# Performance work log

Measured on AMD Instinct MI355X. Metric: run time of the kernel, lower is better.

The kernel has to match this reference:

```python
import jax, jax.numpy as jnp
import numpy as np

EPS_NORM = 1e-6
CLAMP_HI = 1.0 - 1e-6
NEG_INF = -1e30


def _cbrt_pos(x):
    # numerically safe x**(1/3) for x >= 0 (matches exp2(log2(x)/3) in the kernel)
    safe = jnp.where(x > 0, x, 1.0)
    return jnp.where(x > 0, safe ** (1.0 / 3.0), 0.0)


def _pow23_pos(x):
    # relu(x)**(2/3), safe at 0 (matches exp2(log2(max(x,0))*2/3))
    y = jnp.maximum(x, 0.0)
    safe = jnp.where(y > 0, y, 1.0)
    return jnp.where(y > 0, safe ** (2.0 / 3.0), 0.0)


def setup_inputs() -> dict:
    key = jax.random.key(0)
    kq, kk, kv, ks, kd = jax.random.split(key, 5)
    b, h, hkv, s, d = 2, 32, 8, 1024, 64
    return {
        "q": jax.random.normal(kq, (b, h, s, d), dtype=jnp.float32),
        "k": jax.random.normal(kk, (b, hkv, s, d), dtype=jnp.float32),
        "v": jax.random.normal(kv, (b, hkv, s, d), dtype=jnp.float32),
        "src": jax.random.normal(ks, (b, hkv, s), dtype=jnp.float32),
        "dest": jax.random.normal(kd, (b, hkv, s), dtype=jnp.float32),
    }


def reference(q, k, v, src, dest):
    # Preprocessing exactly as in chunked_decay():
    kn = k / (jnp.sqrt(jnp.sum(k * k, axis=-1, keepdims=True)) + EPS_NORM)
    s_gate = _cbrt_pos(jax.nn.sigmoid(src))    # sigmoid(src)**(1/3), [b,hk,S]
    d_gate = _cbrt_pos(jax.nn.sigmoid(dest))   # sigmoid(dest)**(1/3), [b,hk,S]

    # affinity[i,j] = relu(k_i . k_j)**(2/3) * dest_i**(1/3) * src_j**(1/3)
    aff = _pow23_pos(jnp.einsum("bhid,bhjd->bhij", kn, kn))
    aff = aff * d_gate[..., :, None] * s_gate[..., None, :]

    # per-pair log decay, strictly lower-triangular (i > j, as in the kernel mask)
    logdec = jnp.log1p(-jnp.clip(aff, 0.0, CLAMP_HI))
    S = q.shape[2]
    idx = jnp.arange(S)
    strict = idx[:, None] > idx[None, :]
    logdec = jnp.where(strict, logdec, 0.0)

    # cumulative decay seen by query i for key j: sum over j < i' < i (exclusive cumsum over i)
    D = jnp.cumsum(logdec, axis=2) - logdec  # [b,hk,S_i,S_j]

    # GQA: expand kv heads to query heads
    g = q.shape[1] // k.shape[1]
    kq_ = jnp.repeat(kn, g, axis=1)
    vq_ = jnp.repeat(v, g, axis=1)
    Dq_ = jnp.repeat(D, g, axis=1)

    # decay-gated causal softmax attention: logits = q.k + cumulative log-decay
    logits = jnp.einsum("bhid,bhjd->bhij", q, kq_) + Dq_
    causal = idx[:, None] >= idx[None, :]
    logits = jnp.where(causal, logits, NEG_INF)
    att = jax.nn.softmax(logits, axis=-1)
    out = jnp.einsum("bhij,bhjd->bhid", att, vq_)
    return out
```

## Files before the change

### kernel.cpp

```cpp
#include <hip/hip_runtime.h>
#include <hip/hip_bf16.h>
#include <math.h>

#define S_LEN 1024
#define DH 64
#define NB 2
#define NHQ 32
#define NHKV 8
#define NHEADS (NB*NHKV)
#define NTILE 16
#define NTRI 136
#define NEG_INF -1e30f
#define LOG2E 1.44269504088896340736f

using bf16x8 = __attribute__((ext_vector_type(8))) __bf16;
using f32x4  = __attribute__((ext_vector_type(4))) float;
using ushort4_t = __attribute__((ext_vector_type(4))) unsigned short;

__device__ inline unsigned short f2bf(float f){
  unsigned int u = __float_as_uint(f);
  unsigned int r = (u + 0x7FFFu + ((u >> 16) & 1u)) >> 16;
  return (unsigned short)r;
}
__device__ inline unsigned short f2bf_hw(float f){
  return __builtin_bit_cast(unsigned short, __float2bfloat16(f));
}

__device__ inline void gload16(const void* g, void* l){
  __builtin_amdgcn_global_load_lds(
      (const __attribute__((address_space(1))) void*)g,
      (__attribute__((address_space(3))) void*)l, 16, 0, 0);
}

__global__ __launch_bounds__(256) void k_prep(const float* __restrict__ q,
                                              const float* __restrict__ k,
                                              const float* __restrict__ v,
                                              const float* __restrict__ src,
                                              const float* __restrict__ dest,
                                              unsigned short* __restrict__ qb,
                                              unsigned short* __restrict__ knb,
                                              unsigned short* __restrict__ vT,
                                              float* __restrict__ sg,
                                              float* __restrict__ dg){
  __shared__ float tile[64][65];
  int bid = blockIdx.x;
  if (bid < 4096){
    int base = (bid*256 + threadIdx.x)*4;
    float4 qv = *(const float4*)(q + base);
    ushort4_t o;
    o[0] = f2bf_hw(qv.x*LOG2E); o[1] = f2bf_hw(qv.y*LOG2E);
    o[2] = f2bf_hw(qv.z*LOG2E); o[3] = f2bf_hw(qv.w*LOG2E);
    *(ushort4_t*)(qb + base) = o;
  } else if (bid < 4128){
    int e = ((bid - 4096)*256 + threadIdx.x)*4;
    if (e < NHEADS*S_LEN){
      float4 dv = *(const float4*)(dest + e);
      float4 og;
      #pragma unroll
      for (int i = 0; i < 4; ++i){
        float x = (i==0)?dv.x:(i==1)?dv.y:(i==2)?dv.z:dv.w;
        float s = 1.f/(1.f + __expf(-x));
        float g = (s > 0.f) ? exp2f(log2f(s)*(1.f/3.f)) : 0.f;
        if (i==0) og.x=g; else if (i==1) og.y=g; else if (i==2) og.z=g; else og.w=g;
      }
      *(float4*)(dg + e) = og;
    } else {
      int e2 = e - NHEADS*S_LEN;
      float4 sv = *(const float4*)(src + e2);
      float4 og;
      #pragma unroll
      for (int i = 0; i < 4; ++i){
        float x = (i==0)?sv.x:(i==1)?sv.y:(i==2)?sv.z:sv.w;
        float s = 1.f/(1.f + __expf(-x));
        float g = (s > 0.f) ? exp2f(log2f(s)*(1.f/3.f)) : 0.f;
        if (i==0) og.x=g; else if (i==1) og.y=g; else if (i==2) og.z=g; else og.w=g;
      }
      *(float4*)(sg + e2) = og;
    }
  } else if (bid < 8224){
    int row  = (bid - 4128)*4 + (threadIdx.x >> 6);
    int lane = threadIdx.x & 63;
    size_t idx = (size_t)row*DH + lane;
    float x = k[idx];
    float ss = x*x;
    #pragma unroll
    for (int off = 32; off > 0; off >>= 1) ss += __shfl_xor(ss, off);
    float r = x / (sqrtf(ss) + 1e-6f);
    knb[idx] = f2bf(r);
  } else {
    int vb = bid - 8224;
    int bh = vb >> 4;
    int jt = vb & 15;
    int j0 = jt*64;
    int tid = threadIdx.x;
    int c = tid & 63, r4 = tid >> 6;
    const float* vbp = v + ((size_t)bh << 16);
    #pragma unroll
    for (int p = 0; p < 16; ++p){
      int j = p*4 + r4;
      tile[j][c] = vbp[(size_t)(j0 + j)*DH + c];
    }
    __syncthreads();
    unsigned short* ob = vT + ((size_t)bh << 16);
    #pragma unroll
    for (int p = 0; p < 16; ++p){
      int dd = p*4 + r4;
      ob[(size_t)dd*S_LEN + j0 + c] = f2bf_hw(tile[c][dd]);
    }
  }
}

__global__ __launch_bounds__(256) void k_t16(const unsigned short* __restrict__ knh,
                                             const float* __restrict__ dg,
                                             const float* __restrict__ sg,
                                             float* __restrict__ T16){
  __shared__ unsigned short Ah[4096], Bh[4096];
  int head = blockIdx.x / NTRI;
  int t    = blockIdx.x % NTRI;
  int ti = 0;
  while ((ti+1)*(ti+2)/2 <= t) ti++;
  int tj = t - ti*(ti+1)/2;
  int i0 = ti*64, j0 = tj*64;
  const unsigned short* Hp = knh + (size_t)head*S_LEN*DH;
  int w = threadIdx.x >> 6, lane = threadIdx.x & 63;
  int g16 = lane >> 4, l16 = lane & 15;

  int rsub = lane >> 3;
  int cisw = ((lane & 7) ^ rsub) * 8;
  int s0 = (w*8 + rsub)*64   + cisw;
  int s1 = ((w+4)*8 + rsub)*64 + cisw;
  int l0 = w*512, l1 = (w+4)*512;
  {
    const unsigned short* ha = Hp + (size_t)i0*DH;
    gload16(ha + s0, Ah + l0);  gload16(ha + s1, Ah + l1);
    if (ti != tj){
      const unsigned short* hb = Hp + (size_t)j0*DH;
      gload16(hb + s0, Bh + l0);  gload16(hb + s1, Bh + l1);
    }
  }
  __syncthreads();
  const unsigned short* bhp = (ti == tj) ? Ah : Bh;

  int c0 = g16 ^ (l16 & 7);
  int e0 = l16*64 + c0*8;
  int e1 = l16*64 + (c0 ^ 4)*8;

  bf16x8 ah[2];
  ah[0] = *(const bf16x8*)(Ah + w*1024 + e0);
  ah[1] = *(const bf16x8*)(Ah + w*1024 + e1);

  f32x4 sc[4];
  #pragma unroll
  for (int n = 0; n < 4; ++n) sc[n] = (f32x4){0.f,0.f,0.f,0.f};
  #pragma unroll
  for (int n = 0; n < 4; ++n){
    bf16x8 bh0 = *(const bf16x8*)(bhp + n*1024 + e0);
    bf16x8 bh1 = *(const bf16x8*)(bhp + n*1024 + e1);
    sc[n] = __builtin_amdgcn_mfma_f32_16x16x32_bf16(ah[0], bh0, sc[n], 0, 0, 0);
    sc[n] = __builtin_amdgcn_mfma_f32_16x16x32_bf16(ah[1], bh1, sc[n], 0, 0, 0);
  }

  float dgv[4], sgv[4];
  #pragma unroll
  for (int r = 0; r < 4; ++r) dgv[r] = dg[head*S_LEN + i0 + w*16 + g16*4 + r];
  #pragma unroll
  for (int n = 0; n < 4; ++n) sgv[n] = sg[head*S_LEN + j0 + n*16 + l16];

  float tot[4];
  #pragma unroll
  for (int n = 0; n < 4; ++n){
    float s = 0.f;
    #pragma unroll
    for (int r = 0; r < 4; ++r){
      int gi = i0 + w*16 + g16*4 + r;
      int gj = j0 + n*16 + l16;
      float x = sc[n][r];
      float aff = (x > 0.f) ? exp2f(__log2f(x)*(2.f/3.f)) : 0.f;
      aff *= dgv[r]*sgv[n];
      float ld = __log2f(1.f - fminf(aff, 1.0f - 1e-6f));
      s += (gi > gj) ? ld : 0.f;
    }
    tot[n] = s;
  }
  float wt[4];
  #pragma unroll
  for (int n = 0; n < 4; ++n){
    float t0 = __shfl(tot[n], l16);
    float t1 = __shfl(tot[n], 16 + l16);
    float t2 = __shfl(tot[n], 32 + l16);
    float t3 = __shfl(tot[n], 48 + l16);
    wt[n] = t0 + t1 + t2 + t3;
  }
  float sel = (g16 == 0) ? wt[0] : (g16 == 1) ? wt[1] : (g16 == 2) ? wt[2] : wt[3];
  T16[((size_t)head*64 + ti*4 + w)*S_LEN + j0 + g16*16 + l16] = sel;
}

__global__ __launch_bounds__(256) void k_cpre16(const float* __restrict__ T16,
                                                float* __restrict__ Cpre16){
  __shared__ float tot[4][64];
  int head = blockIdx.x >> 4;
  int cb   = blockIdx.x & 15;
  int c    = threadIdx.x >> 6;
  int ci   = threadIdx.x & 63;
  int col  = cb*64 + ci;
  int tjc  = cb;
  float loc[16];
  float run = 0.f;
  #pragma unroll
  for (int i = 0; i < 16; ++i){
    int gg = c*16 + i;
    loc[i] = run;
    if ((gg >> 2) >= tjc) run += T16[((size_t)head*64 + gg)*S_LEN + col];
  }
  tot[c][ci] = run;
  __syncthreads();
  float base = 0.f;
  #pragma unroll
  for (int cc = 0; cc < 3; ++cc)
    if (cc < c) base += tot[cc][ci];
  #pragma unroll
  for (int i = 0; i < 16; ++i){
    int gg = c*16 + i;
    Cpre16[((size_t)head*64 + gg)*S_LEN + col] = base + loc[i];
  }
}

__global__ __launch_bounds__(256, 3) void k_attn(const unsigned short* __restrict__ qb,
                                              const unsigned short* __restrict__ knb,
                                              const unsigned short* __restrict__ vT,
                                              const float* __restrict__ Cpre16,
                                              const float* __restrict__ dg,
                                              const float* __restrict__ sg,
                                              float* __restrict__ out){
  __shared__ unsigned short kts[2][4096];
  __shared__ unsigned short vts[2][4096];
  __shared__ unsigned short plds[4096];
  __shared__ float biasT[2][64][20];

  int xcd   = blockIdx.x & 7;
  int inner = blockIdx.x >> 3;
  int kv    = (xcd << 1) | (inner & 1);
  int i16   = 63 - (inner >> 1);
  int w     = threadIdx.x >> 6;
  int lane  = threadIdx.x & 63;
  int g16 = lane >> 4, l16 = lane & 15;
  int i0   = i16*16;
  int njt  = (i16 >> 2) + 1;
  int head = kv;
  int b = kv >> 3, gh = kv & 7;
  int bh = b*32 + gh*4 + w;

  const unsigned short* Kp = knb + (size_t)head*S_LEN*DH;
  const unsigned short* Vp = vT  + (size_t)head*DH*S_LEN;
  const unsigned short* Qp = qb  + ((size_t)bh*S_LEN + i0)*DH;
  const float*          Cp = Cpre16 + ((size_t)head*64 + i16)*S_LEN;

  int rsub = lane >> 3;
  int cisw = ((lane & 7) ^ rsub) * 8;
  int kg0 = (w*8 + rsub)*64   + cisw;
  int kg1 = ((w+4)*8 + rsub)*64 + cisw;
  int vg0 = (w*8 + rsub)*1024 + cisw;
  int vg1 = ((w+4)*8 + rsub)*1024 + cisw;
  int kl0 = w*512;
  int kl1 = (w+4)*512;

  int c0 = g16 ^ (l16 & 7);
  int e0 = l16*64 + c0*8;
  int e1 = l16*64 + (c0 ^ 4)*8;
  int hi = l16 >> 3, lo = l16 & 7;
  unsigned short* pw = plds + w*1024;

  unsigned short* pp[16];
  #pragma unroll
  for (int n = 0; n < 4; ++n)
    #pragma unroll
    for (int r = 0; r < 4; ++r){
      int row = g16*4 + r;
      pp[n*4 + r] = pw + row*64 + (((2*n + hi) ^ (row & 7))*8) + lo;
    }

  bf16x8 aq[2];
  aq[0] = *(const bf16x8*)(Qp + (size_t)l16*DH + g16*8);
  aq[1] = *(const bf16x8*)(Qp + (size_t)l16*DH + 32 + g16*8);
  bf16x8 ahK[2];
  {
    size_t ro = (size_t)(i0 + l16)*DH + g16*8;
    ahK[0] = *(const bf16x8*)(Kp + ro);
    ahK[1] = *(const bf16x8*)(Kp + ro + 32);
  }
  float dgw[4];
  #pragma unroll
  for (int r = 0; r < 4; ++r) dgw[r] = dg[head*S_LEN + i0 + g16*4 + r];

  auto STAGE = [&](int bb, int jtile){
    const unsigned short* ks = Kp + (size_t)jtile*(64*DH);
    const unsigned short* vs = Vp + (size_t)jtile*64;
    gload16(ks + kg0, &kts[bb][kl0]);
    gload16(ks + kg1, &kts[bb][kl1]);
    gload16(vs + vg0, &vts[bb][kl0]);
    gload16(vs + vg1, &vts[bb][kl1]);
  };

  auto BIAS = [&](int jt, int buf){
    int colw = jt*64 + (w << 4) + l16;
    float sgv_o = sg[head*S_LEN + colw];
    float cp_o  = Cp[colw];
    const unsigned short* hrow = Kp + (size_t)colw*DH;
    bf16x8 bh0 = *(const bf16x8*)(hrow + g16*8);
    bf16x8 bh1 = *(const bf16x8*)(hrow + 32 + g16*8);
    f32x4 bd = (f32x4){0.f,0.f,0.f,0.f};
    bd = __builtin_amdgcn_mfma_f32_16x16x32_bf16(ahK[0], bh0, bd, 0, 0, 0);
    bd = __builtin_amdgcn_mfma_f32_16x16x32_bf16(ahK[1], bh1, bd, 0, 0, 0);
    float pre[4];
    float s = 0.f;
    #pragma unroll
    for (int r = 0; r < 4; ++r){
      float x = bd[r];
      float aff = (x > 0.f) ? exp2f(__log2f(x)*(2.f/3.f)) : 0.f;
      aff *= dgw[r]*sgv_o;
      float ld = __log2f(1.f - fminf(aff, 1.0f - 1e-6f));
      ld = ((i0 + g16*4 + r) > colw) ? ld : 0.f;
      pre[r] = s; s += ld;
    }
    float t0 = __shfl(s, l16);
    float t1 = __shfl(s, 16 + l16);
    float t2 = __shfl(s, 32 + l16);
    float offg = (g16 > 0 ? t0 : 0.f) + (g16 > 1 ? t1 : 0.f) + (g16 > 2 ? t2 : 0.f);
    f32x4 st;
    #pragma unroll
    for (int r = 0; r < 4; ++r) st[r] = cp_o + offg + pre[r];
    *(f32x4*)&biasT[buf][(w << 4) + l16][g16*4] = st;
  };

  f32x4 oacc[4];
  float m[4], ssum[4];
  #pragma unroll
  for (int n = 0; n < 4; ++n) oacc[n] = (f32x4){0.f,0.f,0.f,0.f};
  #pragma unroll
  for (int r = 0; r < 4; ++r){ m[r] = NEG_INF; ssum[r] = 0.f; }

  auto SM_PV = [&](f32x4* sc, const unsigned short* vcur){
    float mx[4];
    #pragma unroll
    for (int r = 0; r < 4; ++r)
      mx[r] = fmaxf(fmaxf(sc[0][r], sc[1][r]), fmaxf(sc[2][r], sc[3][r]));
    #pragma unroll
    for (int off = 8; off >= 1; off >>= 1)
      #pragma unroll
      for (int r = 0; r < 4; ++r)
        mx[r] = fmaxf(mx[r], __shfl_xor(mx[r], off));
    float dmax = fmaxf(fmaxf(mx[0]-m[0], mx[1]-m[1]), fmaxf(mx[2]-m[2], mx[3]-m[3]));
    if (__any(dmax > 8.f)){
      #pragma unroll
      for (int r = 0; r < 4; ++r){
        float mn = fmaxf(m[r], mx[r]);
        float scale = exp2f(m[r] - mn);
        m[r] = mn;
        ssum[r] *= scale;
        #pragma unroll
        for (int n = 0; n < 4; ++n) oacc[n][r] *= scale;
      }
    }
    #pragma unroll
    for (int n = 0; n < 4; ++n){
      #pragma unroll
      for (int r = 0; r < 4; ++r){
        float pv = exp2f(sc[n][r] - m[r]);
        ssum[r] += pv;
        *pp[n*4 + r] = f2bf_hw(pv);
      }
    }
    bf16x8 pa0 = *(const bf16x8*)(pw + e0);
    bf16x8 pa1 = *(const bf16x8*)(pw + e1);
    __builtin_amdgcn_s_setprio(1);
    #pragma unroll
    for (int n = 0; n < 4; ++n){
      bf16x8 bv = *(const bf16x8*)(vcur + n*1024 + e0);
      oacc[n] = __builtin_amdgcn_mfma_f32_16x16x32_bf16(pa0, bv, oacc[n], 0, 0, 0);
    }
    #pragma unroll
    for (int n = 0; n < 4; ++n){
      bf16x8 bv = *(const bf16x8*)(vcur + n*1024 + e1);
      oacc[n] = __builtin_amdgcn_mfma_f32_16x16x32_bf16(pa1, bv, oacc[n], 0, 0, 0);
    }
    __builtin_amdgcn_s_setprio(0);
  };

  STAGE(0, 0);
  BIAS(0, 0);
  __syncthreads();

  int cur = 0, nb = 0;
  for (int jt = 0; jt < njt - 1; ++jt){
    const unsigned short* kcur = &kts[cur][0];
    const unsigned short* vcur = &vts[cur][0];

    STAGE(cur ^ 1, jt + 1);

    f32x4 sc[4];
    #pragma unroll
    for (int n = 0; n < 4; ++n) sc[n] = (f32x4){0.f,0.f,0.f,0.f};
    __builtin_amdgcn_s_setprio(1);
    #pragma unroll
    for (int n = 0; n < 4; ++n){
      bf16x8 bk0 = *(const bf16x8*)(kcur + n*1024 + e0);
      bf16x8 bk1 = *(const bf16x8*)(kcur + n*1024 + e1);
      sc[n] = __builtin_amdgcn_mfma_f32_16x16x32_bf16(aq[0], bk0, sc[n], 0, 0, 0);
      sc[n] = __builtin_amdgcn_mfma_f32_16x16x32_bf16(aq[1], bk1, sc[n], 0, 0, 0);
    }
    __builtin_amdgcn_s_setprio(0);

    BIAS(jt + 1, nb ^ 1);

    #pragma unroll
    for (int n = 0; n < 4; ++n){
      f32x4 bvv = *(const f32x4*)&biasT[nb][n*16 + l16][g16*4];
      #pragma unroll
      for (int r = 0; r < 4; ++r) sc[n][r] += bvv[r];
    }

    SM_PV(sc, vcur);

    __syncthreads();
    cur ^= 1; nb ^= 1;
  }

  {
    const unsigned short* kcur = &kts[cur][0];
    const unsigned short* vcur = &vts[cur][0];

    f32x4 sc[4];
    #pragma unroll
    for (int n = 0; n < 4; ++n) sc[n] = (f32x4){0.f,0.f,0.f,0.f};
    __builtin_amdgcn_s_setprio(1);
    #pragma unroll
    for (int n = 0; n < 4; ++n){
      bf16x8 bk0 = *(const bf16x8*)(kcur + n*1024 + e0);
      bf16x8 bk1 = *(const bf16x8*)(kcur + n*1024 + e1);
      sc[n] = __builtin_amdgcn_mfma_f32_16x16x32_bf16(aq[0], bk0, sc[n], 0, 0, 0);
      sc[n] = __builtin_amdgcn_mfma_f32_16x16x32_bf16(aq[1], bk1, sc[n], 0, 0, 0);
    }
    __builtin_amdgcn_s_setprio(0);

    int lim = (i16 & 3) << 4;
    #pragma unroll
    for (int n = 0; n < 4; ++n){
      f32x4 bvv = *(const f32x4*)&biasT[nb][n*16 + l16][g16*4];
      #pragma unroll
      for (int r = 0; r < 4; ++r){
        int row = g16*4 + r;
        int col = n*16 + l16;
        sc[n][r] = (col <= lim + row) ? (sc[n][r] + bvv[r]) : NEG_INF;
      }
    }

    SM_PV(sc, vcur);
  }

  #pragma unroll
  for (int off = 8; off >= 1; off >>= 1)
    #pragma unroll
    for (int r = 0; r < 4; ++r) ssum[r] += __shfl_xor(ssum[r], off);
  float* Op = out + ((size_t)bh*S_LEN + i0)*DH;
  #pragma unroll
  for (int n = 0; n < 4; ++n)
    #pragma unroll
    for (int r = 0; r < 4; ++r)
      Op[(size_t)(g16*4 + r)*DH + n*16 + l16] = oacc[n][r] / ssum[r];
}

extern "C" void kernel_launch(void* const* d_in, const int* in_sizes, int n_in,
                              void* d_out, int out_size, void* d_ws, size_t ws_size,
                              hipStream_t stream){
  const float* q    = (const float*)d_in[0];
  const float* k    = (const float*)d_in[1];
  const float* v    = (const float*)d_in[2];
  const float* src  = (const float*)d_in[3];
  const float* dest = (const float*)d_in[4];
  float* out = (float*)d_out;

  char* w = (char*)d_ws;
  unsigned short* qb   = (unsigned short*)w;
  unsigned short* knb  = (unsigned short*)(w + (size_t)(8u  << 20));
  unsigned short* vT   = (unsigned short*)(w + (size_t)(10u << 20));
  float*          dg   = (float*)(w + (size_t)(12u << 20));
  float*          sg   = (float*)(w + (size_t)(12u << 20) + 65536);
  float*          T16  = (float*)(w + (size_t)(13u << 20));
  float*          Cpre = (float*)(w + (size_t)(17u << 20));

  k_prep   <<<dim3(8480), dim3(256), 0, stream>>>(q, k, v, src, dest, qb, knb, vT, sg, dg);
  k_t16    <<<dim3(NHEADS*NTRI), dim3(256), 0, stream>>>(knb, dg, sg, T16);
  k_cpre16 <<<dim3(NHEADS*16), dim3(256), 0, stream>>>(T16, Cpre);
  k_attn   <<<dim3(NB*NHKV*64), dim3(256), 0, stream>>>(qb, knb, vT, Cpre, dg, sg, out);
}
```

Baseline: 70.87 us.

## Single-buffer K tile with extra barrier and swizzle bias LDS layout

After: 71.24 us. About the same (+0.5%).

```diff
diff --git a/kernel.cpp b/kernel.cpp
--- a/kernel.cpp
+++ b/kernel.cpp
@@ -232,10 +232,10 @@
                                               const float* __restrict__ dg,
                                               const float* __restrict__ sg,
                                               float* __restrict__ out){
-  __shared__ unsigned short kts[2][4096];
+  __shared__ unsigned short kts[4096];
   __shared__ unsigned short vts[2][4096];
   __shared__ unsigned short plds[4096];
-  __shared__ float biasT[2][64][20];
+  __shared__ float biasT[2][64][16];
 
   int xcd   = blockIdx.x & 7;
   int inner = blockIdx.x >> 3;
@@ -269,6 +269,7 @@
   int e1 = l16*64 + (c0 ^ 4)*8;
   int hi = l16 >> 3, lo = l16 & 7;
   unsigned short* pw = plds + w*1024;
+  int bsw = (g16 ^ (l16 & 3)) << 2;
 
   unsigned short* pp[16];
   #pragma unroll
@@ -292,11 +293,13 @@
   #pragma unroll
   for (int r = 0; r < 4; ++r) dgw[r] = dg[head*S_LEN + i0 + g16*4 + r];
 
-  auto STAGE = [&](int bb, int jtile){
+  auto STAGE_K = [&](int jtile){
     const unsigned short* ks = Kp + (size_t)jtile*(64*DH);
+    gload16(ks + kg0, kts + kl0);
+    gload16(ks + kg1, kts + kl1);
+  };
+  auto STAGE_V = [&](int bb, int jtile){
     const unsigned short* vs = Vp + (size_t)jtile*64;
-    gload16(ks + kg0, &kts[bb][kl0]);
-    gload16(ks + kg1, &kts[bb][kl1]);
     gload16(vs + vg0, &vts[bb][kl0]);
     gload16(vs + vg1, &vts[bb][kl1]);
   };
@@ -329,7 +332,7 @@
     f32x4 st;
     #pragma unroll
     for (int r = 0; r < 4; ++r) st[r] = cp_o + offg + pre[r];
-    *(f32x4*)&biasT[buf][(w << 4) + l16][g16*4] = st;
+    *(f32x4*)&biasT[buf][(w << 4) + l16][bsw] = st;
   };
 
   f32x4 oacc[4];
@@ -386,16 +389,17 @@
     __builtin_amdgcn_s_setprio(0);
   };
 
-  STAGE(0, 0);
+  STAGE_K(0);
+  STAGE_V(0, 0);
   BIAS(0, 0);
   __syncthreads();
 
   int cur = 0, nb = 0;
-  for (int jt = 0; jt < njt - 1; ++jt){
-    const unsigned short* kcur = &kts[cur][0];
+  for (int jt = 0; jt < njt; ++jt){
+    bool last = (jt == njt - 1);
     const unsigned short* vcur = &vts[cur][0];
 
-    STAGE(cur ^ 1, jt + 1);
+    if (!last) STAGE_V(cur ^ 1, jt + 1);
 
     f32x4 sc[4];
     #pragma unroll
@@ -403,58 +407,45 @@
     __builtin_amdgcn_s_setprio(1);
     #pragma unroll
     for (int n = 0; n < 4; ++n){
-      bf16x8 bk0 = *(const bf16x8*)(kcur + n*1024 + e0);
-      bf16x8 bk1 = *(const bf16x8*)(kcur + n*1024 + e1);
+      bf16x8 bk0 = *(const bf16x8*)(kts + n*1024 + e0);
+      bf16x8 bk1 = *(const bf16x8*)(kts + n*1024 + e1);
       sc[n] = __builtin_amdgcn_mfma_f32_16x16x32_bf16(aq[0], bk0, sc[n], 0, 0, 0);
       sc[n] = __builtin_amdgcn_mfma_f32_16x16x32_bf16(aq[1], bk1, sc[n], 0, 0, 0);
     }
     __builtin_amdgcn_s_setprio(0);
 
-    BIAS(jt + 1, nb ^ 1);
-
-    #pragma unroll
-    for (int n = 0; n < 4; ++n){
-      f32x4 bvv = *(const f32x4*)&biasT[nb][n*16 + l16][g16*4];
-      #pragma unroll
-      for (int r = 0; r < 4; ++r) sc[n][r] += bvv[r];
+    __syncthreads();
+
+    if (!last){
+      STAGE_K(jt + 1);
+      BIAS(jt + 1, nb ^ 1);
+    }
+
+    if (last){
+      int lim = (i16 & 3) << 4;
+      #pragma unroll
+      for (int n = 0; n < 4; ++n){
+        f32x4 bvv = *(const f32x4*)&biasT[nb][n*16 + l16][bsw];
+        #pragma unroll
+        for (int r = 0; r < 4; ++r){
+          int row = g16*4 + r;
+          int col = n*16 + l16;
+          sc[n][r] = (col <= lim + row) ? (sc[n][r] + bvv[r]) : NEG_INF;
+        }
+      }
+    } else {
+      #pragma unroll
+      for (int n = 0; n < 4; ++n){
+        f32x4 bvv = *(const f32x4*)&biasT[nb][n*16 + l16][bsw];
+        #pragma unroll
+        for (int r = 0; r < 4; ++r) sc[n][r] += bvv[r];
+      }
     }
 
     SM_PV(sc, vcur);
 
     __syncthreads();
     cur ^= 1; nb ^= 1;
-  }
-
-  {
-    const unsigned short* kcur = &kts[cur][0];
-    const unsigned short* vcur = &vts[cur][0];
-
-    f32x4 sc[4];
-    #pragma unroll
-    for (int n = 0; n < 4; ++n) sc[n] = (f32x4){0.f,0.f,0.f,0.f};
-    __builtin_amdgcn_s_setprio(1);
-    #pragma unroll
-    for (int n = 0; n < 4; ++n){
-      bf16x8 bk0 = *(const bf16x8*)(kcur + n*1024 + e0);
-      bf16x8 bk1 = *(const bf16x8*)(kcur + n*1024 + e1);
-      sc[n] = __builtin_amdgcn_mfma_f32_16x16x32_bf16(aq[0], bk0, sc[n], 0, 0, 0);
-      sc[n] = __builtin_amdgcn_mfma_f32_16x16x32_bf16(aq[1], bk1, sc[n], 0, 0, 0);
-    }
-    __builtin_amdgcn_s_setprio(0);
-
-    int lim = (i16 & 3) << 4;
-    #pragma unroll
-    for (int n = 0; n < 4; ++n){
-      f32x4 bvv = *(const f32x4*)&biasT[nb][n*16 + l16][g16*4];
-      #pragma unroll
-      for (int r = 0; r < 4; ++r){
-        int row = g16*4 + r;
-        int col = n*16 + l16;
-        sc[n][r] = (col <= lim + row) ? (sc[n][r] + bvv[r]) : NEG_INF;
-      }
-    }
-
-    SM_PV(sc, vcur);
   }
 
   #pragma unroll
```
